# Performance work log

Hardware: AMD Instinct MI355X
Metric: run time of the kernel (lower is better)

Reference implementation:

```python
import jax, jax.numpy as jnp
import numpy as np

B, N, D = 32, 540, 512
H = 8
DH = D // H
MAX_LEN = 540
POS_CLIP = MAX_LEN - 1


def setup_inputs() -> dict:
    key = jax.random.key(0)
    ks = jax.random.split(key, 12)
    s = 0.02
    inp = {
        "query": jax.random.normal(ks[0], (B, N, D), dtype=jnp.float32),
        "Wq": jax.random.normal(ks[1], (D, D), dtype=jnp.float32) * s,
        "bq": jnp.zeros((D,), jnp.float32),
        "Wk": jax.random.normal(ks[2], (D, D), dtype=jnp.float32) * s,
        "bk": jnp.zeros((D,), jnp.float32),
        "Wv": jax.random.normal(ks[3], (D, D), dtype=jnp.float32) * s,
        "bv": jnp.zeros((D,), jnp.float32),
        "Wh": jax.random.normal(ks[4], (D, D), dtype=jnp.float32) * s,
        "bh": jnp.zeros((D,), jnp.float32),
        "pos_k": jax.random.uniform(ks[5], (2 * POS_CLIP + 1, DH), dtype=jnp.float32, minval=-0.05, maxval=0.05),
        "gamma": jnp.ones((D,), jnp.float32),
        "beta": jnp.zeros((D,), jnp.float32),
        "valid_len": jax.random.randint(ks[6], (B,), 1, N + 1, dtype=jnp.int32),
    }
    return inp


def _split_heads(x):
    # [B, N, D] -> [H*B, N, DH], head-major on axis 0 (matches tf.concat(tf.split(x,H,-1),0))
    return x.reshape(B, N, H, DH).transpose(2, 0, 1, 3).reshape(H * B, N, DH)


def reference(query, Wq, bq, Wk, bk, Wv, bv, Wh, bh, pos_k, gamma, beta, valid_len):
    q = _split_heads(query @ Wq + bq)  # [HB, N, DH]
    k = _split_heads(query @ Wk + bk)
    v = _split_heads(query @ Wv + bv)

    QK = jnp.einsum("xqd,xkd->xqk", q, k)  # [HB, N, N]

    # relative position bias (Shaw et al. 2018)
    rel = jnp.arange(N)[None, :] - jnp.arange(N)[:, None]
    rel = jnp.clip(rel, -POS_CLIP, POS_CLIP) + POS_CLIP
    pos_enc_k = pos_k[rel]  # [N, N, DH]
    QR = jnp.einsum("xqd,qkd->xqk", q, pos_enc_k)

    attn = (QK + QR) / jnp.sqrt(jnp.float32(DH))

    # key-side sequence mask, broadcast over heads and query rows
    key_mask = jnp.arange(N)[None, :] < valid_len[:, None]  # [B, N]
    key_mask = jnp.tile(key_mask[:, None, :], (H, N, 1))  # [HB, N, N]
    attn = jnp.where(key_mask, attn, jnp.float32(-1e12))
    attn = jax.nn.softmax(attn, axis=-1)

    out = jnp.einsum("xqk,xkd->xqd", attn, v)  # [HB, N, DH]
    out = out.reshape(H, B, N, DH).transpose(1, 2, 0, 3).reshape(B, N, D)
    out = out @ Wh + bh
    out = out + query

    # layer norm over last axis
    mean = jnp.mean(out, axis=-1, keepdims=True)
    var = jnp.mean(jnp.square(out - mean), axis=-1, keepdims=True)
    normalized = (out - mean) * jax.lax.rsqrt(var + 1e-7)
    return gamma * normalized + beta
```

## Files before the change

kernel.cpp:

```cpp
#include <hip/hip_runtime.h>
#include <hip/hip_bf16.h>

typedef __hip_bfloat16 bf16;

#define NB 32
#define NSEQ 540
#define ND 512
#define NH 8
#define NDH 64
#define NHB 256
#define NM 17280
#define NPOS 1079
#define VTP 544

typedef __bf16 v8bf __attribute__((ext_vector_type(8)));
typedef float f32x4 __attribute__((ext_vector_type(4)));

union U8 {
  uint4 u;
  unsigned short s[8];
  v8bf v;
};

__device__ __forceinline__ unsigned short f2b(float x) {
  union { float f; unsigned u; } c;
  c.f = x;
  const unsigned r = c.u + 0x7fffu + ((c.u >> 16) & 1u);
  return (unsigned short)(r >> 16);
}

__device__ __forceinline__ float b2f16(unsigned short s) {
  return __uint_as_float(((unsigned)s) << 16);
}

__device__ __forceinline__ void bar_lds() {
  asm volatile("s_waitcnt lgkmcnt(0)\n\ts_barrier" ::: "memory");
}

__device__ __forceinline__ int xcd_swz(int p, int total) {
  const int g = p >> 5, r = p & 31;
  return ((g << 5) + 32 <= total) ? ((g << 5) + ((r & 7) << 2) + (r >> 3)) : p;
}

__device__ __forceinline__ void gl_lds16(const unsigned short* g,
                                         unsigned short* l) {
  __builtin_amdgcn_global_load_lds(
      (const __attribute__((address_space(1))) unsigned int*)g,
      (__attribute__((address_space(3))) unsigned int*)l, 16, 0, 0);
}

__device__ __forceinline__ void cvt16(const float* __restrict__ p,
                                      unsigned short* __restrict__ dst) {
  unsigned short s[16];
#pragma unroll
  for (int i = 0; i < 4; i++) {
    const float4 v = *(const float4*)(p + i * 4);
    s[i * 4 + 0] = f2b(v.x);
    s[i * 4 + 1] = f2b(v.y);
    s[i * 4 + 2] = f2b(v.z);
    s[i * 4 + 3] = f2b(v.w);
  }
  *(uint4*)dst = *(uint4*)s;
  *(uint4*)(dst + 8) = *(uint4*)(s + 8);
}

__global__ __launch_bounds__(256) void prep(const float* __restrict__ x,
                                            unsigned short* __restrict__ xb,
                                            const float* __restrict__ pos,
                                            unsigned short* __restrict__ posb) {
  const int blk = blockIdx.x;
  if (blk < 4320) {
    const int i = blk * 256 + threadIdx.x;
    const float4 a = *(const float4*)(x + (size_t)i * 8);
    const float4 b = *(const float4*)(x + (size_t)i * 8 + 4);
    unsigned short s[8];
    s[0] = f2b(a.x); s[1] = f2b(a.y); s[2] = f2b(a.z); s[3] = f2b(a.w);
    s[4] = f2b(b.x); s[5] = f2b(b.y); s[6] = f2b(b.z); s[7] = f2b(b.w);
    *(uint4*)(xb + (size_t)i * 8) = *(uint4*)s;
  } else {
    const int i = (blk - 4320) * 256 + threadIdx.x;
    if (i < NPOS * NDH) posb[i] = f2b(pos[i]);
  }
}

__global__ __launch_bounds__(256) void wcvt(
    const float* __restrict__ Wq, const float* __restrict__ Wk,
    const float* __restrict__ Wv, const float* __restrict__ Wh,
    unsigned short* __restrict__ Wt) {
  __shared__ unsigned short T[64][72];
  const int tid = threadIdx.x;
  const int sel = blockIdx.z;
  const float* W = (sel == 0) ? Wq : (sel == 1) ? Wk : (sel == 2) ? Wv : Wh;
  unsigned short* out = Wt + (size_t)sel * ND * ND;
  const int k0 = blockIdx.x * 64, n0 = blockIdx.y * 64;
  const int r = tid >> 2, g = tid & 3;
  cvt16(W + (size_t)(k0 + r) * ND + n0 + g * 16, &T[r][g * 16]);
  __syncthreads();
  unsigned short s[16];
#pragma unroll
  for (int j = 0; j < 16; j++) s[j] = T[g * 16 + j][r];
  unsigned short* dst = out + (size_t)(n0 + r) * ND + k0 + g * 16;
  *(uint4*)dst = *(uint4*)s;
  *(uint4*)(dst + 8) = *(uint4*)(s + 8);
}

#define GEMM_CORE_B16(APTR)                                                       \
  {                                                                               \
    const int lrow = lane >> 2;                                                   \
    const int lc8 = (lane & 3) * 8;                                               \
    const int arow = 32 * w + lrow;                   \
    unsigned short* lA0 = &As[0][0] + (size_t)(2 * w) * 512;                      \
    unsigned short* lB0 = &Bs[0][0] + (size_t)(2 * w) * 512;                      \
    for (int k0 = 0; k0 < 512; k0 += 32) {                                        \
      __syncthreads();                                                            \
      gl_lds16(APTR + (size_t)(m0 + arow) * ND + k0 + lc8, lA0);                  \
      gl_lds16(APTR + (size_t)(m0 + arow + 16) * ND + k0 + lc8, lA0 + 512);       \
      gl_lds16(Bt + (size_t)(n0 + arow) * ND + k0 + lc8, lB0);                    \
      gl_lds16(Bt + (size_t)(n0 + arow + 16) * ND + k0 + lc8, lB0 + 512);         \
      __syncthreads();                                                            \
      U8 af[4], bfr[4];                                                           \
      _Pragma("unroll")                                                           \
      for (int mi = 0; mi < 4; mi++)                                              \
        af[mi].u = *(const uint4*)&As[wr * 64 + mi * 16 + l15][quad * 8];         \
      _Pragma("unroll")                                                           \
      for (int ni = 0; ni < 4; ni++)                                              \
        bfr[ni].u = *(const uint4*)&Bs[wc * 64 + ni * 16 + l15][quad * 8];        \
      _Pragma("unroll")                                                           \
      for (int mi = 0; mi < 4; mi++)                                              \
        _Pragma("unroll")                                                         \
        for (int ni = 0; ni < 4; ni++)                                            \
          acc[mi][ni] = __builtin_amdgcn_mfma_f32_16x16x32_bf16(                  \
              af[mi].v, bfr[ni].v, acc[mi][ni], 0, 0, 0);                         \
    }                                                                             \
  }

__global__ __launch_bounds__(256, 3) void qkv_mfma(
    const unsigned short* __restrict__ Xb, const unsigned short* __restrict__ Wt,
    const float* __restrict__ bq, const float* __restrict__ bk,
    const float* __restrict__ bv,
    bf16* __restrict__ qh, bf16* __restrict__ kh, bf16* __restrict__ vt) {
  __shared__ unsigned short As[128][32];
  __shared__ unsigned short Bs[128][32];
  const int tid = threadIdx.x;
  const int phys = blockIdx.x + (blockIdx.y << 2) + 540 * blockIdx.z;
  const int W = xcd_swz(phys, 1620);
  const int sel = W / 540;
  const int rem = W - sel * 540;
  const int m0 = (rem >> 2) * 128, n0 = (rem & 3) * 128;
  const unsigned short* Bt = Wt + (size_t)sel * ND * ND;
  const float* bias = (sel == 0) ? bq : (sel == 1) ? bk : bv;
  const int lane = tid & 63, w = tid >> 6;
  const int wr = w & 1, wc = w >> 1;
  const int l15 = lane & 15, quad = lane >> 4;

  f32x4 acc[4][4];
#pragma unroll
  for (int mi = 0; mi < 4; mi++)
#pragma unroll
    for (int ni = 0; ni < 4; ni++) acc[mi][ni] = (f32x4){0.f, 0.f, 0.f, 0.f};

  GEMM_CORE_B16(Xb)

  if (sel != 2) {
    unsigned short* o = (unsigned short*)((sel == 0) ? qh : kh);
#pragma unroll
    for (int mi = 0; mi < 4; mi++) {
      const int m = m0 + wr * 64 + mi * 16 + quad * 4;
      const int bidx = m / NSEQ;
      const int seq0 = m - bidx * NSEQ;
#pragma unroll
      for (int ni = 0; ni < 4; ni++) {
        const int n = n0 + wc * 64 + ni * 16 + l15;
        const int h = n >> 6, dh = n & 63;
        const float bsv = bias[n];
        const size_t base = (((size_t)(h * NB + bidx)) * NSEQ + seq0) * NDH + dh;
#pragma unroll
        for (int i = 0; i < 4; i++)
          o[base + (size_t)i * NDH] = f2b(acc[mi][ni][i] + bsv);
      }
    }
  } else {
    unsigned short* o = (unsigned short*)vt;
#pragma unroll
    for (int mi = 0; mi < 4; mi++) {
      const int m = m0 + wr * 64 + mi * 16 + quad * 4;
      const int bidx = m / NSEQ;
      const int seq0 = m - bidx * NSEQ;
#pragma unroll
      for (int ni = 0; ni < 4; ni++) {
        const int n = n0 + wc * 64 + ni * 16 + l15;
        const int h = n >> 6, dh = n & 63;
        const float bsv = bias[n];
        unsigned short pk[4];
#pragma unroll
        for (int i = 0; i < 4; i++) pk[i] = f2b(acc[mi][ni][i] + bsv);
        *(uint2*)(o + (((size_t)(h * NB + bidx)) * NDH + dh) * VTP + seq0) =
            *(uint2*)pk;
      }
    }
  }
}

__global__ __launch_bounds__(256, 3) void out_mfma(
    const unsigned short* __restrict__ ctxb, const unsigned short* __restrict__ Wht,
    const float* __restrict__ bh, const float* __restrict__ query,
    float* __restrict__ tmp) {
  __shared__ unsigned short As[128][32];
  __shared__ unsigned short Bs[128][32];
  const int tid = threadIdx.x;
  const unsigned short* Bt = Wht;
  const int phys = blockIdx.x + (blockIdx.y << 2);
  const int W = xcd_swz(phys, 540);
  const int m0 = (W >> 2) * 128, n0 = (W & 3) * 128;
  const int lane = tid & 63, w = tid >> 6;
  const int wr = w & 1, wc = w >> 1;
  const int l15 = lane & 15, quad = lane >> 4;

  f32x4 acc[4][4];
#pragma unroll
  for (int mi = 0; mi < 4; mi++)
#pragma unroll
    for (int ni = 0; ni < 4; ni++) acc[mi][ni] = (f32x4){0.f, 0.f, 0.f, 0.f};

  GEMM_CORE_B16(ctxb)

#pragma unroll
  for (int mi = 0; mi < 4; mi++) {
    const int m = m0 + wr * 64 + mi * 16 + quad * 4;
#pragma unroll
    for (int ni = 0; ni < 4; ni++) {
      const int n = n0 + wc * 64 + ni * 16 + l15;
      const float bsv = bh[n];
#pragma unroll
      for (int i = 0; i < 4; i++) {
        const size_t off = (size_t)(m + i) * ND + n;
        tmp[off] = acc[mi][ni][i] + bsv + query[off];
      }
    }
  }
}

#define PW 584

__global__ __launch_bounds__(256, 6) void attn(
    const bf16* __restrict__ qh, const bf16* __restrict__ kh,
    const bf16* __restrict__ vt, const unsigned short* __restrict__ posb,
    const int* __restrict__ vlen, bf16* __restrict__ ctx) {
  __shared__ unsigned short P[16][PW];
  __shared__ float Tt[16][84];
  __shared__ float red4[16][4];
  __shared__ float sinv[16];

  const int tid = threadIdx.x;
  const int lane = tid & 63;
  const int w = tid >> 6;
  const int l15 = lane & 15;
  const int quad = lane >> 4;
  const int qb = blockIdx.x;
  const int x = blockIdx.y;
  const int b = x & 31, h = x >> 5;
  const int q0 = qb * 16;
  const int valid = vlen[b];
  const int NT = (valid + 63) >> 6;
  const int NC = (valid + 31) >> 5;
  const bf16* qbase = qh + (size_t)x * NSEQ * NDH;
  const unsigned short* kbase = (const unsigned short*)(kh + (size_t)x * NSEQ * NDH);
  const unsigned short* vbase = (const unsigned short*)(vt + (size_t)x * NDH * VTP);

  U8 aq0, aq1;
  {
    const int q = q0 + l15;
    if (q < NSEQ) {
      aq0.u = *(const uint4*)(qbase + (size_t)q * NDH + quad * 8);
      aq1.u = *(const uint4*)(qbase + (size_t)q * NDH + 32 + quad * 8);
    } else {
      aq0.u = make_uint4(0, 0, 0, 0);
      aq1.u = make_uint4(0, 0, 0, 0);
    }
  }

  U8 ck0, ck1, cp0, cp1, ce0, ce1;
  {
    const int key = w * 16 + l15;
    ck0.u = *(const uint4*)(kbase + (size_t)key * NDH + quad * 8);
    ck1.u = *(const uint4*)(kbase + (size_t)key * NDH + 32 + quad * 8);
    const long pr = (long)(524 - q0 + w * 16 + l15);
    cp0.u = *(const uint4*)(posb + pr * NDH + quad * 8);
    cp1.u = *(const uint4*)(posb + pr * NDH + 32 + quad * 8);
    if (w == 0) {
      const long pr2 = (long)(524 - q0 + 64 + l15);
      ce0.u = *(const uint4*)(posb + pr2 * NDH + quad * 8);
      ce1.u = *(const uint4*)(posb + pr2 * NDH + 32 + quad * 8);
    }
  }

  float pmax[4];
#pragma unroll
  for (int i = 0; i < 4; i++) pmax[i] = -1e30f;

  for (int kt = 0; kt < NT; kt++) {
    U8 nk0, nk1, np0, np1, ne0, ne1;
    if (kt < NT - 1) {
      const int k1 = kt * 64 + 64;
      const int key = k1 + w * 16 + l15;
      nk0.u = *(const uint4*)(kbase + (size_t)key * NDH + quad * 8);
      nk1.u = *(const uint4*)(kbase + (size_t)key * NDH + 32 + quad * 8);
      const long pr = (long)(k1 - q0 + 524 + w * 16 + l15);
      np0.u = *(const uint4*)(posb + pr * NDH + quad * 8);
      np1.u = *(const uint4*)(posb + pr * NDH + 32 + quad * 8);
      if (w == 0) {
        const long pr2 = (long)(k1 - q0 + 524 + 64 + l15);
        ne0.u = *(const uint4*)(posb + pr2 * NDH + quad * 8);
        ne1.u = *(const uint4*)(posb + pr2 * NDH + 32 + quad * 8);
      }
    }

    f32x4 accqk = {0.f, 0.f, 0.f, 0.f};
    accqk = __builtin_amdgcn_mfma_f32_16x16x32_bf16(aq0.v, ck0.v, accqk, 0, 0, 0);
    accqk = __builtin_amdgcn_mfma_f32_16x16x32_bf16(aq1.v, ck1.v, accqk, 0, 0, 0);
    f32x4 accT = {0.f, 0.f, 0.f, 0.f};
    accT = __builtin_amdgcn_mfma_f32_16x16x32_bf16(aq0.v, cp0.v, accT, 0, 0, 0);
    accT = __builtin_amdgcn_mfma_f32_16x16x32_bf16(aq1.v, cp1.v, accT, 0, 0, 0);
    f32x4 accT2 = {0.f, 0.f, 0.f, 0.f};
    if (w == 0) {
      accT2 = __builtin_amdgcn_mfma_f32_16x16x32_bf16(aq0.v, ce0.v, accT2, 0, 0, 0);
      accT2 = __builtin_amdgcn_mfma_f32_16x16x32_bf16(aq1.v, ce1.v, accT2, 0, 0, 0);
    }

    bar_lds();
#pragma unroll
    for (int i = 0; i < 4; i++) Tt[quad * 4 + i][w * 16 + l15] = accT[i];
    if (w == 0) {
#pragma unroll
      for (int i = 0; i < 4; i++) Tt[quad * 4 + i][64 + l15] = accT2[i];
    }
    bar_lds();
    {
      const int k0 = kt * 64;
      const int kk = w * 16 + l15;
      const bool cm = (k0 + kk) < valid;
#pragma unroll
      for (int i = 0; i < 4; i++) {
        const int qq = quad * 4 + i;
        const float v = (accqk[i] + Tt[qq][kk + 15 - qq]) * 0.125f;
        P[qq][k0 + kk] = f2b(v);
        if (cm) pmax[i] = fmaxf(pmax[i], v);
      }
    }
    ck0 = nk0; ck1 = nk1; cp0 = np0; cp1 = np1;
    if (w == 0) { ce0 = ne0; ce1 = ne1; }
  }

#pragma unroll
  for (int m = 1; m < 16; m <<= 1) {
#pragma unroll
    for (int i = 0; i < 4; i++)
      pmax[i] = fmaxf(pmax[i], __shfl_xor(pmax[i], m, 16));
  }
  if (l15 == 0) {
#pragma unroll
    for (int i = 0; i < 4; i++) red4[quad * 4 + i][w] = pmax[i];
  }

  const int dh = w * 16 + l15;
  const unsigned short* vrow = vbase + (size_t)dh * VTP;
  U8 cv;
  cv.u = *(const uint4*)(vrow + quad * 8);

  bar_lds();

  {
    const int r = tid >> 4, c = tid & 15;
    const float4 rm = *(const float4*)red4[r];
    const float rowmax = fmaxf(fmaxf(rm.x, rm.y), fmaxf(rm.z, rm.w));
    const int nv = (valid + 7) >> 3;
    float sl = 0.f;
    for (int ch = c; ch < nv; ch += 16) {
      const uint4 u = *(const uint4*)&P[r][ch * 8];
      unsigned ue[4];
#pragma unroll
      for (int jj = 0; jj < 4; jj++) {
        const unsigned uu = ((const unsigned*)&u)[jj];
        const float lo = __uint_as_float(uu << 16);
        const float hi = __uint_as_float(uu & 0xffff0000u);
        float el = __expf(lo - rowmax);
        float eh = __expf(hi - rowmax);
        const int cb = ch * 8 + jj * 2;
        el = (cb < valid) ? el : 0.f;
        eh = (cb + 1 < valid) ? eh : 0.f;
        sl += el + eh;
        ue[jj] = (unsigned)f2b(el) | ((unsigned)f2b(eh) << 16);
      }
      *(uint4*)&P[r][ch * 8] = *(const uint4*)ue;
    }
    for (int ch = c; ch < 72; ch += 16) {
      if (ch >= nv) *(uint4*)&P[r][ch * 8] = make_uint4(0, 0, 0, 0);
    }
#pragma unroll
    for (int m = 1; m < 16; m <<= 1) sl += __shfl_xor(sl, m, 16);
    if (c == 0) sinv[r] = 1.f / sl;
  }
  bar_lds();

  f32x4 acco = {0.f, 0.f, 0.f, 0.f};
  for (int ci = 0; ci < NC; ci++) {
    U8 nv_;
    if (ci + 1 < NC) nv_.u = *(const uint4*)(vrow + (ci + 1) * 32 + quad * 8);
    U8 ap;
    ap.u = *(const uint4*)&P[l15][ci * 32 + quad * 8];
    acco = __builtin_amdgcn_mfma_f32_16x16x32_bf16(ap.v, cv.v, acco, 0, 0, 0);
    cv = nv_;
  }
  unsigned short* ob = (unsigned short*)ctx;
#pragma unroll
  for (int i = 0; i < 4; i++) {
    const int q = q0 + quad * 4 + i;
    if (q < NSEQ) {
      ob[((size_t)b * NSEQ + q) * ND + h * NDH + dh] =
          f2b(acco[i] * sinv[quad * 4 + i]);
    }
  }
}

__global__ __launch_bounds__(256) void lnorm(
    const float* __restrict__ tmp, const float* __restrict__ gamma,
    const float* __restrict__ beta, float* __restrict__ out) {
  const int w = threadIdx.x >> 6, lane = threadIdx.x & 63;
  const int row = blockIdx.x * 4 + w;
  const size_t base = (size_t)row * 512 + lane * 8;
  const float4 a = *(const float4*)(tmp + base);
  const float4 b = *(const float4*)(tmp + base + 4);

  float s = a.x + a.y + a.z + a.w + b.x + b.y + b.z + b.w;
#pragma unroll
  for (int m = 1; m < 64; m <<= 1) s += __shfl_xor(s, m, 64);
  const float mean = s * (1.f / 512.f);

  float d[8] = {a.x - mean, a.y - mean, a.z - mean, a.w - mean,
                b.x - mean, b.y - mean, b.z - mean, b.w - mean};
  float v = 0.f;
#pragma unroll
  for (int i = 0; i < 8; i++) v += d[i] * d[i];
#pragma unroll
  for (int m = 1; m < 64; m <<= 1) v += __shfl_xor(v, m, 64);
  const float rstd = rsqrtf(v * (1.f / 512.f) + 1e-7f);

  const int col = lane * 8;
  const float4 g0 = *(const float4*)(gamma + col);
  const float4 g1 = *(const float4*)(gamma + col + 4);
  const float4 be0 = *(const float4*)(beta + col);
  const float4 be1 = *(const float4*)(beta + col + 4);
  float4 o0, o1;
  o0.x = d[0] * rstd * g0.x + be0.x;
  o0.y = d[1] * rstd * g0.y + be0.y;
  o0.z = d[2] * rstd * g0.z + be0.z;
  o0.w = d[3] * rstd * g0.w + be0.w;
  o1.x = d[4] * rstd * g1.x + be1.x;
  o1.y = d[5] * rstd * g1.y + be1.y;
  o1.z = d[6] * rstd * g1.z + be1.z;
  o1.w = d[7] * rstd * g1.w + be1.w;
  *(float4*)(out + base) = o0;
  *(float4*)(out + base + 4) = o1;
}

extern "C" void kernel_launch(void* const* d_in, const int* in_sizes, int n_in,
                              void* d_out, int out_size, void* d_ws, size_t ws_size,
                              hipStream_t stream) {
  const float* query = (const float*)d_in[0];
  const float* Wq = (const float*)d_in[1];
  const float* bq = (const float*)d_in[2];
  const float* Wk = (const float*)d_in[3];
  const float* bk = (const float*)d_in[4];
  const float* Wv = (const float*)d_in[5];
  const float* bv = (const float*)d_in[6];
  const float* Wh = (const float*)d_in[7];
  const float* bh = (const float*)d_in[8];
  const float* pos = (const float*)d_in[9];
  const float* gamma = (const float*)d_in[10];
  const float* beta = (const float*)d_in[11];
  const int* vlen = (const int*)d_in[12];

  bf16* ws = (bf16*)d_ws;
  const size_t QSZ = (size_t)NHB * NSEQ * NDH;
  const size_t VSZ = (size_t)NHB * NDH * VTP;
  bf16* qh = ws;
  bf16* kh = ws + QSZ;
  bf16* vt = ws + 2 * QSZ;
  unsigned short* posb = (unsigned short*)(ws + 2 * QSZ + VSZ);
  unsigned short* Wtb = posb + (size_t)NPOS * NDH;
  unsigned short* Xb = (unsigned short*)d_out;
  bf16* ctx = (bf16*)d_out;
  float* tmp = (float*)d_ws;
  (void)ws_size;

  prep<<<dim3(4590), 256, 0, stream>>>(query, Xb, pos, posb);
  wcvt<<<dim3(8, 8, 4), 256, 0, stream>>>(Wq, Wk, Wv, Wh, Wtb);
  qkv_mfma<<<dim3(4, 135, 3), 256, 0, stream>>>(Xb, Wtb, bq, bk, bv, qh, kh, vt);
  attn<<<dim3(34, 256), 256, 0, stream>>>(qh, kh, vt, posb, vlen, ctx);
  out_mfma<<<dim3(4, 135), 256, 0, stream>>>((const unsigned short*)ctx,
                                             Wtb + 3 * (size_t)ND * ND, bh, query, tmp);
  lnorm<<<dim3(4320), 256, 0, stream>>>(tmp, gamma, beta, (float*)d_out);
}
```

Before: 306.4 us.

## Double-buffer GEMM LDS tiles and transpose attention score MFMA layout

The shared GEMM core now double-buffers the A/B LDS tiles, prefetching the next k-slice while MFMAs run on the current one, so each iteration needs one barrier instead of two. In the attention kernel the QK and position MFMAs swap operands so each lane holds four consecutive keys of one query row. That allows vectorized LDS stores of the position tile and packed 4-element P writes, and replaces the 16-lane shuffle reduction with two cross-quad shuffles. Double buffering doubles GEMM LDS use (32KB per block), which may reduce occupancy under launch_bounds(256,3).

```diff
diff --git a/kernel.cpp b/kernel.cpp
--- a/kernel.cpp
+++ b/kernel.cpp
@@ -20,6 +20,11 @@
   uint4 u;
   unsigned short s[8];
   v8bf v;
+};
+
+union U2 {
+  uint2 u;
+  unsigned short s[4];
 };
 
 __device__ __forceinline__ unsigned short f2b(float x) {
@@ -109,28 +114,38 @@
     const int lrow = lane >> 2;                                                   \
     const int lc8 = (lane & 3) * 8;                                               \
     const int arow = 32 * w + lrow;                   \
-    unsigned short* lA0 = &As[0][0] + (size_t)(2 * w) * 512;                      \
-    unsigned short* lB0 = &Bs[0][0] + (size_t)(2 * w) * 512;                      \
-    for (int k0 = 0; k0 < 512; k0 += 32) {                                        \
-      __syncthreads();                                                            \
-      gl_lds16(APTR + (size_t)(m0 + arow) * ND + k0 + lc8, lA0);                  \
-      gl_lds16(APTR + (size_t)(m0 + arow + 16) * ND + k0 + lc8, lA0 + 512);       \
-      gl_lds16(Bt + (size_t)(n0 + arow) * ND + k0 + lc8, lB0);                    \
-      gl_lds16(Bt + (size_t)(n0 + arow + 16) * ND + k0 + lc8, lB0 + 512);         \
-      __syncthreads();                                                            \
+    const unsigned short* ga = APTR + (size_t)(m0 + arow) * ND + lc8;             \
+    const unsigned short* gb = Bt + (size_t)(n0 + arow) * ND + lc8;               \
+    gl_lds16(ga, &As[0][(2 * w) * 512]);                                          \
+    gl_lds16(ga + 16 * ND, &As[0][(2 * w) * 512 + 512]);                          \
+    gl_lds16(gb, &Bs[0][(2 * w) * 512]);                                          \
+    gl_lds16(gb + 16 * ND, &Bs[0][(2 * w) * 512 + 512]);                          \
+    __syncthreads();                                                              \
+    for (int t = 0; t < 16; t++) {                                                \
+      const int cur = t & 1;                                                      \
+      if (t < 15) {                                                               \
+        const int k1 = (t + 1) * 32;                                              \
+        gl_lds16(ga + k1, &As[cur ^ 1][(2 * w) * 512]);                           \
+        gl_lds16(ga + k1 + 16 * ND, &As[cur ^ 1][(2 * w) * 512 + 512]);           \
+        gl_lds16(gb + k1, &Bs[cur ^ 1][(2 * w) * 512]);                           \
+        gl_lds16(gb + k1 + 16 * ND, &Bs[cur ^ 1][(2 * w) * 512 + 512]);           \
+      }                                                                           \
       U8 af[4], bfr[4];                                                           \
       _Pragma("unroll")                                                           \
       for (int mi = 0; mi < 4; mi++)                                              \
-        af[mi].u = *(const uint4*)&As[wr * 64 + mi * 16 + l15][quad * 8];         \
+        af[mi].u = *(const uint4*)&As[cur][(wr * 64 + mi * 16 + l15) * 32 +       \
+                                           quad * 8];                             \
       _Pragma("unroll")                                                           \
       for (int ni = 0; ni < 4; ni++)                                              \
-        bfr[ni].u = *(const uint4*)&Bs[wc * 64 + ni * 16 + l15][quad * 8];        \
+        bfr[ni].u = *(const uint4*)&Bs[cur][(wc * 64 + ni * 16 + l15) * 32 +      \
+                                            quad * 8];                            \
       _Pragma("unroll")                                                           \
       for (int mi = 0; mi < 4; mi++)                                              \
         _Pragma("unroll")                                                         \
         for (int ni = 0; ni < 4; ni++)                                            \
           acc[mi][ni] = __builtin_amdgcn_mfma_f32_16x16x32_bf16(                  \
               af[mi].v, bfr[ni].v, acc[mi][ni], 0, 0, 0);                         \
+      __syncthreads();                                                            \
     }                                                                             \
   }
 
@@ -139,8 +154,8 @@
     const float* __restrict__ bq, const float* __restrict__ bk,
     const float* __restrict__ bv,
     bf16* __restrict__ qh, bf16* __restrict__ kh, bf16* __restrict__ vt) {
-  __shared__ unsigned short As[128][32];
-  __shared__ unsigned short Bs[128][32];
+  __shared__ unsigned short As[2][4096];
+  __shared__ unsigned short Bs[2][4096];
   const int tid = threadIdx.x;
   const int phys = blockIdx.x + (blockIdx.y << 2) + 540 * blockIdx.z;
   const int W = xcd_swz(phys, 1620);
@@ -205,8 +220,8 @@
     const unsigned short* __restrict__ ctxb, const unsigned short* __restrict__ Wht,
     const float* __restrict__ bh, const float* __restrict__ query,
     float* __restrict__ tmp) {
-  __shared__ unsigned short As[128][32];
-  __shared__ unsigned short Bs[128][32];
+  __shared__ unsigned short As[2][4096];
+  __shared__ unsigned short Bs[2][4096];
   const int tid = threadIdx.x;
   const unsigned short* Bt = Wht;
   const int phys = blockIdx.x + (blockIdx.y << 2);
@@ -294,9 +309,7 @@
     }
   }
 
-  float pmax[4];
-#pragma unroll
-  for (int i = 0; i < 4; i++) pmax[i] = -1e30f;
+  float pmax1 = -1e30f;
 
   for (int kt = 0; kt < NT; kt++) {
     U8 nk0, nk1, np0, np1, ne0, ne1;
@@ -316,51 +329,44 @@
     }
 
     f32x4 accqk = {0.f, 0.f, 0.f, 0.f};
-    accqk = __builtin_amdgcn_mfma_f32_16x16x32_bf16(aq0.v, ck0.v, accqk, 0, 0, 0);
-    accqk = __builtin_amdgcn_mfma_f32_16x16x32_bf16(aq1.v, ck1.v, accqk, 0, 0, 0);
+    accqk = __builtin_amdgcn_mfma_f32_16x16x32_bf16(ck0.v, aq0.v, accqk, 0, 0, 0);
+    accqk = __builtin_amdgcn_mfma_f32_16x16x32_bf16(ck1.v, aq1.v, accqk, 0, 0, 0);
     f32x4 accT = {0.f, 0.f, 0.f, 0.f};
-    accT = __builtin_amdgcn_mfma_f32_16x16x32_bf16(aq0.v, cp0.v, accT, 0, 0, 0);
-    accT = __builtin_amdgcn_mfma_f32_16x16x32_bf16(aq1.v, cp1.v, accT, 0, 0, 0);
+    accT = __builtin_amdgcn_mfma_f32_16x16x32_bf16(cp0.v, aq0.v, accT, 0, 0, 0);
+    accT = __builtin_amdgcn_mfma_f32_16x16x32_bf16(cp1.v, aq1.v, accT, 0, 0, 0);
     f32x4 accT2 = {0.f, 0.f, 0.f, 0.f};
     if (w == 0) {
-      accT2 = __builtin_amdgcn_mfma_f32_16x16x32_bf16(aq0.v, ce0.v, accT2, 0, 0, 0);
-      accT2 = __builtin_amdgcn_mfma_f32_16x16x32_bf16(aq1.v, ce1.v, accT2, 0, 0, 0);
+      accT2 = __builtin_amdgcn_mfma_f32_16x16x32_bf16(ce0.v, aq0.v, accT2, 0, 0, 0);
+      accT2 = __builtin_amdgcn_mfma_f32_16x16x32_bf16(ce1.v, aq1.v, accT2, 0, 0, 0);
     }
 
     bar_lds();
-#pragma unroll
-    for (int i = 0; i < 4; i++) Tt[quad * 4 + i][w * 16 + l15] = accT[i];
-    if (w == 0) {
-#pragma unroll
-      for (int i = 0; i < 4; i++) Tt[quad * 4 + i][64 + l15] = accT2[i];
-    }
+    *(f32x4*)&Tt[l15][w * 16 + quad * 4] = accT;
+    if (w == 0) *(f32x4*)&Tt[l15][64 + quad * 4] = accT2;
     bar_lds();
     {
       const int k0 = kt * 64;
-      const int kk = w * 16 + l15;
-      const bool cm = (k0 + kk) < valid;
+      const int cb = w * 16 + quad * 4;
+      const int jb = cb + 15 - l15;
+      U2 pk;
+      float pm = -1e30f;
 #pragma unroll
       for (int i = 0; i < 4; i++) {
-        const int qq = quad * 4 + i;
-        const float v = (accqk[i] + Tt[qq][kk + 15 - qq]) * 0.125f;
-        P[qq][k0 + kk] = f2b(v);
-        if (cm) pmax[i] = fmaxf(pmax[i], v);
+        const float v = (accqk[i] + Tt[l15][jb + i]) * 0.125f;
+        pk.s[i] = f2b(v);
+        const bool cm = (k0 + cb + i) < valid;
+        pm = fmaxf(pm, cm ? v : -1e30f);
       }
+      *(uint2*)&P[l15][k0 + cb] = pk.u;
+      pmax1 = fmaxf(pmax1, pm);
     }
     ck0 = nk0; ck1 = nk1; cp0 = np0; cp1 = np1;
     if (w == 0) { ce0 = ne0; ce1 = ne1; }
   }
 
-#pragma unroll
-  for (int m = 1; m < 16; m <<= 1) {
-#pragma unroll
-    for (int i = 0; i < 4; i++)
-      pmax[i] = fmaxf(pmax[i], __shfl_xor(pmax[i], m, 16));
-  }
-  if (l15 == 0) {
-#pragma unroll
-    for (int i = 0; i < 4; i++) red4[quad * 4 + i][w] = pmax[i];
-  }
+  pmax1 = fmaxf(pmax1, __shfl_xor(pmax1, 16, 64));
+  pmax1 = fmaxf(pmax1, __shfl_xor(pmax1, 32, 64));
+  if (quad == 0) red4[l15][w] = pmax1;
 
   const int dh = w * 16 + l15;
   const unsigned short* vrow = vbase + (size_t)dh * VTP;
```

After: 309.9 us. About the same (+1.1%).
